# Optimization experiments

Measured on AMD Instinct MI355X. Metric: run time of the kernel, lower is better.

Reference implementation:

```python
import jax, jax.numpy as jnp
import numpy as np

B = 2            # batch size
GRID = 256       # BEV grid H = W
M = 30000        # number of pillars (voxels)
NPTS = 200000    # number of points
IN_C = 16
VOXEL = 0.4      # voxel_size[:2]
PC_MIN = -51.2   # pc_range[:2]
DS = 2           # prod(ds_layer_strides)


def _bn(x, g, b):
    # eval-mode BatchNorm with running_mean=0, running_var=1 (eps absorbed into g)
    return x * g + b


def _conv(x, k, stride):
    # 3x3 conv, padding=1 (spconv SparseConv2d / SubMConv2d with pad k//2), NHWC
    return jax.lax.conv_general_dilated(
        x, k, (stride, stride), ((1, 1), (1, 1)),
        dimension_numbers=('NHWC', 'HWIO', 'NHWC'))


def _active_mask(occ, stride):
    # active output sites of a sparse conv = any active input in the 3x3 receptive field
    pooled = jax.lax.reduce_window(occ, -jnp.inf, jax.lax.max,
                                   (1, 3, 3, 1), (1, stride, stride, 1),
                                   ((0, 0), (1, 1), (1, 1), (0, 0)))
    return (pooled > 0).astype(occ.dtype)


def _forward(features, pfn_w0, pfn_g0, pfn_b0, pfn_w1, pfn_g1, pfn_b1,
             b1_kd, b1_gd, b1_bd, b1_k1, b1_g1, b1_b1, b1_k2, b1_g2, b1_b2,
             b2_kd, b2_gd, b2_bd, b2_k1, b2_g1, b2_b1, b2_k2, b2_g2, b2_b2,
             unq, unq_inv, grid_size):
    # pillar mode: cols 0:2 are xy; convert to (fractional) voxel coordinates
    pos = (features[:, :2] - PC_MIN) / VOXEL  # [N,2] = (px, py)

    # PFN layer 0 (not last): linear(16->16) + BN + ReLU, concat per-pillar max
    h = jax.nn.relu(_bn(features @ pfn_w0, pfn_g0, pfn_b0))            # [N,16]
    hmax = jax.ops.segment_max(h, unq_inv, num_segments=M)             # [M,16]
    h = jnp.concatenate([h, hmax[unq_inv]], axis=1)                    # [N,32]
    # PFN layer 1 (last): linear(32->64) + BN + ReLU
    h = jax.nn.relu(_bn(h @ pfn_w1, pfn_g1, pfn_b1))                   # [N,64]

    # scatter_max pooling points -> pillars
    fv = jax.ops.segment_max(h, unq_inv, num_segments=M)               # [M,64]

    Hn = grid_size
    img = jnp.zeros((B, Hn, Hn, fv.shape[1]), fv.dtype)
    img = img.at[unq[:, 0], unq[:, 1], unq[:, 2]].set(fv)              # dense BEV, NHWC
    occ = jnp.zeros((B, Hn, Hn, 1), fv.dtype)
    occ = occ.at[unq[:, 0], unq[:, 1], unq[:, 2]].set(1.0)

    # block 1: SparseConvBlock(stride=1) + SparseBasicBlock (dense math, masked to active sites)
    occ1 = _active_mask(occ, 1)
    x = jax.nn.relu(_bn(_conv(img, b1_kd, 1), b1_gd, b1_bd)) * occ1
    y = jax.nn.relu(_bn(_conv(x, b1_k1, 1), b1_g1, b1_b1)) * occ1
    y = _bn(_conv(y, b1_k2, 1), b1_g2, b1_b2) * occ1
    x = jax.nn.relu(x + y)

    # block 2: SparseConvBlock(stride=2) + SparseBasicBlock
    occ2 = _active_mask(occ1, 2)
    x = jax.nn.relu(_bn(_conv(x, b2_kd, 2), b2_gd, b2_bd)) * occ2
    y = jax.nn.relu(_bn(_conv(x, b2_k1, 1), b2_g1, b2_b1)) * occ2
    y = _bn(_conv(y, b2_k2, 1), b2_g2, b2_b2) * occ2
    x = jax.nn.relu(x + y)                                             # [B,H/2,W/2,128]

    # bilinear gather at per-point downsampled positions (px -> W axis, py -> H axis)
    bidx = unq[unq_inv, 0]
    px = pos[:, 0] / DS
    py = pos[:, 1] / DS
    Hc, Wc = x.shape[1], x.shape[2]
    x0 = jnp.clip(jnp.floor(px).astype(jnp.int32), 0, Wc - 1)
    x1 = jnp.clip(jnp.floor(px).astype(jnp.int32) + 1, 0, Wc - 1)
    y0 = jnp.clip(jnp.floor(py).astype(jnp.int32), 0, Hc - 1)
    y1 = jnp.clip(jnp.floor(py).astype(jnp.int32) + 1, 0, Hc - 1)
    Ia = x[bidx, y0, x0]
    Ib = x[bidx, y1, x0]
    Ic = x[bidx, y0, x1]
    Id = x[bidx, y1, x1]
    x0f, x1f = x0.astype(px.dtype), x1.astype(px.dtype)
    y0f, y1f = y0.astype(py.dtype), y1.astype(py.dtype)
    wa = ((x1f - px) * (y1f - py))[:, None]
    wb = ((x1f - px) * (py - y0f))[:, None]
    wc = ((px - x0f) * (y1f - py))[:, None]
    wd = ((px - x0f) * (py - y0f))[:, None]
    return Ia * wa + Ib * wb + Ic * wc + Id * wd                       # [N,128]


def setup_inputs() -> dict:
    rng = np.random.default_rng(0)
    d = {}
    d['features'] = jnp.asarray(rng.standard_normal((NPTS, IN_C)).astype(np.float32))
    # unique voxel coords (batch, y, x)
    lin = rng.choice(B * GRID * GRID, size=M, replace=False)
    d['unq'] = jnp.asarray(np.stack([lin // (GRID * GRID), (lin // GRID) % GRID, lin % GRID], 1).astype(np.int32))
    # every pillar gets at least one point
    d['unq_inv'] = jnp.asarray(np.concatenate([np.arange(M), rng.integers(0, M, NPTS - M)]).astype(np.int32))
    d['grid_size'] = GRID

    def w(*s):
        fan = int(np.prod(s[:-1]))
        return jnp.asarray((rng.standard_normal(s) / np.sqrt(fan)).astype(np.float32))

    def g(c):
        return jnp.asarray((0.5 + 0.5 * rng.random(c)).astype(np.float32))

    def bb(c):
        return jnp.asarray((0.1 * rng.standard_normal(c)).astype(np.float32))

    d['pfn_w0'] = w(IN_C, 16); d['pfn_g0'] = g(16); d['pfn_b0'] = bb(16)
    d['pfn_w1'] = w(32, 64);   d['pfn_g1'] = g(64); d['pfn_b1'] = bb(64)
    d['b1_kd'] = w(3, 3, 64, 64);   d['b1_gd'] = g(64);  d['b1_bd'] = bb(64)
    d['b1_k1'] = w(3, 3, 64, 64);   d['b1_g1'] = g(64);  d['b1_b1'] = bb(64)
    d['b1_k2'] = w(3, 3, 64, 64);   d['b1_g2'] = g(64);  d['b1_b2'] = bb(64)
    d['b2_kd'] = w(3, 3, 64, 128);  d['b2_gd'] = g(128); d['b2_bd'] = bb(128)
    d['b2_k1'] = w(3, 3, 128, 128); d['b2_g1'] = g(128); d['b2_b1'] = bb(128)
    d['b2_k2'] = w(3, 3, 128, 128); d['b2_g2'] = g(128); d['b2_b2'] = bb(128)
    return d


def reference(features, unq, unq_inv, grid_size,
              pfn_w0, pfn_g0, pfn_b0, pfn_w1, pfn_g1, pfn_b1,
              b1_kd, b1_gd, b1_bd, b1_k1, b1_g1, b1_b1, b1_k2, b1_g2, b1_b2,
              b2_kd, b2_gd, b2_bd, b2_k1, b2_g1, b2_b1, b2_k2, b2_g2, b2_b2):
    return _forward(features, pfn_w0, pfn_g0, pfn_b0, pfn_w1, pfn_g1, pfn_b1,
                    b1_kd, b1_gd, b1_bd, b1_k1, b1_g1, b1_b1, b1_k2, b1_g2, b1_b2,
                    b2_kd, b2_gd, b2_bd, b2_k1, b2_g1, b2_b1, b2_k2, b2_g2, b2_b2,
                    unq, unq_inv, grid_size)
```

## Files before the change

### kernel.cpp

```cpp
#include <hip/hip_runtime.h>
#include <hip/hip_bf16.h>

#define NPTS    200000
#define MPIL    30000
#define BATCH   2
#define GRID0   256
#define PCMIN   (-51.2f)
#define VOXEL0  (0.4f)
#define NCHUNK  118

#define SLOT_B  ((size_t)16777216)
#define SLOT_F  ((size_t)33554432)

#define W0F 0
#define W1F 256
#define FB1 9216
#define FB2 156672
#define FB3 304128
#define FB4 451584
#define FB5 746496
#define FB6 1336320

#define WS_FLAG 0
#define WS_OCC8 64
#define WS_OCC1 (64 + 131072)
#define WS_OCC2 (64 + 262144)
#define WS_HMAX 393280
#define WS_CNT  2313280
#define WS_OFF  2433280
#define WS_CUR  2553344
#define WS_IDX  2673344
#define WS_LOC  3473344
#define WS_BS   3593344
#define WS_FX   393344

typedef __attribute__((ext_vector_type(8))) short v8s;
typedef __attribute__((ext_vector_type(4))) float f32x4;

static __device__ __forceinline__ float b2f(__hip_bfloat16 v) { return __bfloat162float(v); }
static __device__ __forceinline__ unsigned short f2bbits(float f) {
    __hip_bfloat16 h = __float2bfloat16(f);
    union { __hip_bfloat16 h; unsigned short u; } cv; cv.h = h; return cv.u;
}
static __device__ __forceinline__ float bits2f(unsigned short h) {
    union { unsigned int u; float f; } c; c.u = ((unsigned int)h) << 16; return c.f;
}
static __device__ __forceinline__ float lo2f(unsigned int u) {
    union { unsigned int u; float f; } c; c.u = u << 16; return c.f;
}
static __device__ __forceinline__ float hi2f(unsigned int u) {
    union { unsigned int u; float f; } c; c.u = u & 0xFFFF0000u; return c.f;
}
static __device__ __forceinline__ unsigned int pack2(float a, float b) {
    return (unsigned int)f2bbits(a) | ((unsigned int)f2bbits(b) << 16);
}
static __device__ __forceinline__ void split2(float a, float b, unsigned int& hi, unsigned int& lo) {
    unsigned short ha = f2bbits(a), hb = f2bbits(b);
    hi = (unsigned int)ha | ((unsigned int)hb << 16);
    float ra = a - bits2f(ha);
    float rb = b - bits2f(hb);
    lo = (unsigned int)f2bbits(ra) | ((unsigned int)f2bbits(rb) << 16);
}

static __device__ __forceinline__ float ldf(const void* p, size_t i, int isb) {
    return isb ? b2f(((const __hip_bfloat16*)p)[i]) : ((const float*)p)[i];
}
static __device__ __forceinline__ float4 ld4(const void* p, size_t i, int isb) {
    if (isb) {
        uint2 r = *(const uint2*)((const __hip_bfloat16*)p + i);
        return make_float4(lo2f(r.x), hi2f(r.x), lo2f(r.y), hi2f(r.y));
    }
    return *(const float4*)((const float*)p + i);
}
static __device__ __forceinline__ void st4(void* p, size_t i, int isb, float4 v) {
    if (isb) {
        uint2 pk; pk.x = pack2(v.x, v.y); pk.y = pack2(v.z, v.w);
        *(uint2*)((__hip_bfloat16*)p + i) = pk;
    } else {
        *(float4*)((float*)p + i) = v;
    }
}
static __device__ __forceinline__ void* actptr(void* ob, int slot, int isb) {
    return (char*)ob + (size_t)slot * (isb ? SLOT_B : SLOT_F);
}
static __device__ __forceinline__ float* wpool(void* ob, int isb) {
    return (float*)((char*)ob + 3 * (isb ? SLOT_B : SLOT_F));
}

__global__ void probe_kernel(const unsigned short* __restrict__ g0, int* __restrict__ flag) {
    if (threadIdx.x == 0 && blockIdx.x == 0) {
        int ok = 1;
        for (int i = 0; i < 8; i++) {
            unsigned short u = g0[i];
            if (u < 0x3E00 || u >= 0x4000) ok = 0;
        }
        *flag = ok;
    }
}

__global__ __launch_bounds__(256) void cvt_kernel(const void* __restrict__ src, void* ob,
                                                  int woff, int n, const int* __restrict__ flag) {
    int isb = *flag;
    int i = blockIdx.x * 256 + threadIdx.x;
    if (i < n) wpool(ob, isb)[woff + i] = ldf(src, i, isb);
}

__global__ __launch_bounds__(256) void wfrag_kernel(const void* __restrict__ src, void* ob,
                                                    int fb_bytes, int CIN, int COUT,
                                                    const int* __restrict__ flag)
{
    const int isb = *flag;
    const int cnt = 9 * CIN * COUT;
    int e = blockIdx.x * 256 + threadIdx.x;
    if (e >= cnt) return;
    int i = e & 7;
    int l = (e >> 3) & 63;
    int f = e >> 9;
    int nbn = COUT >> 4, kcn = CIN >> 5;
    int nb = f % nbn;
    int kc = (f / nbn) % kcn;
    int tap = f / (nbn * kcn);
    int ci = kc * 32 + (l >> 4) * 8 + i;
    int co = nb * 16 + (l & 15);
    float wv = ldf(src, (size_t)(tap * CIN + ci) * COUT + co, isb);
    unsigned short h = f2bbits(wv);
    float rem = wv - bits2f(h);
    short* wh = (short*)((char*)ob + 3 * (isb ? SLOT_B : SLOT_F) + fb_bytes);
    wh[e] = (short)h;
    wh[cnt + e] = (short)f2bbits(rem);
}

__global__ __launch_bounds__(256) void hist_kernel(const int* __restrict__ unq_inv,
                                                   int* __restrict__ cnt)
{
    int n = blockIdx.x * 256 + threadIdx.x;
    if (n < NPTS) atomicAdd(&cnt[unq_inv[n]], 1);
}

__global__ __launch_bounds__(256) void scan1_kernel(const int* __restrict__ cnt,
                                                    int* __restrict__ loc,
                                                    int* __restrict__ bs)
{
    __shared__ int s[256];
    const int tid = threadIdx.x;
    const int i = blockIdx.x * 256 + tid;
    int v = (i < MPIL) ? cnt[i] : 0;
    s[tid] = v;
    __syncthreads();
#pragma unroll
    for (int d = 1; d < 256; d <<= 1) {
        int t = (tid >= d) ? s[tid - d] : 0;
        __syncthreads();
        s[tid] += t;
        __syncthreads();
    }
    if (i < MPIL) loc[i] = s[tid] - v;
    if (tid == 255) bs[blockIdx.x] = s[255];
}

__global__ __launch_bounds__(128) void scan2_kernel(int* __restrict__ bs)
{
    __shared__ int s[NCHUNK];
    const int tid = threadIdx.x;
    for (int i = tid; i < NCHUNK; i += 128) s[i] = bs[i];
    __syncthreads();
    if (tid == 0) {
        int acc = 0;
        for (int i = 0; i < NCHUNK; i++) { int t = s[i]; s[i] = acc; acc += t; }
    }
    __syncthreads();
    for (int i = tid; i < NCHUNK; i += 128) bs[i] = s[i];
}

__global__ __launch_bounds__(256) void scan3_kernel(const int* __restrict__ loc,
                                                    const int* __restrict__ bs,
                                                    int* __restrict__ off,
                                                    int* __restrict__ cur)
{
    int i = blockIdx.x * 256 + threadIdx.x;
    if (i < MPIL) {
        int e = loc[i] + bs[blockIdx.x];
        off[i] = e; cur[i] = e;
    }
    if (i == 0) off[MPIL] = NPTS;
}

__global__ __launch_bounds__(256) void fill_kernel(const int* __restrict__ unq_inv,
                                                   int* __restrict__ cur,
                                                   int* __restrict__ idxarr)
{
    int n = blockIdx.x * 256 + threadIdx.x;
    if (n >= NPTS) return;
    int p = unq_inv[n];
    int s = atomicAdd(&cur[p], 1);
    idxarr[s] = n;
}

__global__ __launch_bounds__(256) void pfn0_kernel(
    const void* __restrict__ feat, void* ob, const void* __restrict__ g0,
    const void* __restrict__ b0, const int* __restrict__ flag)
{
    const int isb = *flag;
    int n = blockIdx.x * 256 + threadIdx.x;
    if (n >= NPTS) return;
    const float* w0f = wpool(ob, isb) + W0F;
    void* h0 = actptr(ob, 1, isb);
    float f[16];
#pragma unroll
    for (int i = 0; i < 16; i += 4) {
        float4 v = ld4(feat, (size_t)n * 16 + i, isb);
        f[i] = v.x; f[i + 1] = v.y; f[i + 2] = v.z; f[i + 3] = v.w;
    }
#pragma unroll
    for (int co = 0; co < 16; co += 4) {
        float a0 = 0.f, a1 = 0.f, a2 = 0.f, a3 = 0.f;
#pragma unroll
        for (int ci = 0; ci < 16; ci++) {
            float4 w = *(const float4*)&w0f[ci * 16 + co];
            a0 += f[ci] * w.x; a1 += f[ci] * w.y; a2 += f[ci] * w.z; a3 += f[ci] * w.w;
        }
        float o[4] = { a0, a1, a2, a3 };
#pragma unroll
        for (int k = 0; k < 4; k++) {
            float z = o[k] * ldf(g0, co + k, isb) + ldf(b0, co + k, isb);
            o[k] = fmaxf(z, 0.f);
        }
        st4(h0, (size_t)n * 16 + co, isb, make_float4(o[0], o[1], o[2], o[3]));
    }
}

__global__ __launch_bounds__(256) void hmax_kernel(
    void* ob, const int* __restrict__ off, const int* __restrict__ idxarr,
    float* __restrict__ hmax, const int* __restrict__ flag)
{
    const int isb = *flag;
    int t = blockIdx.x * 256 + threadIdx.x;
    if (t >= MPIL * 16) return;
    int p = t >> 4, ch = t & 15;
    const void* h0 = actptr(ob, 1, isb);
    float m = 0.f;
    int s1 = off[p + 1];
    for (int s = off[p]; s < s1; s++) {
        int n = idxarr[s];
        m = fmaxf(m, ldf(h0, (size_t)n * 16 + ch, isb));
    }
    hmax[t] = m;
}

template<bool BF>
static __device__ __forceinline__ void pfn1p_body(
    void* ob, const float* __restrict__ hmax, const void* __restrict__ g1,
    const void* __restrict__ b1, const int* __restrict__ off,
    const int* __restrict__ idxarr, const int* __restrict__ unq,
    unsigned char* __restrict__ occ)
{
    const int lane = threadIdx.x & 63;
    const int p = (blockIdx.x << 2) + (threadIdx.x >> 6);
    if (p >= MPIL) return;
    const int isb = BF ? 1 : 0;
    const float* w1f = wpool(ob, isb) + W1F;
    const void* h0 = actptr(ob, 1, isb);
    void* img = actptr(ob, 0, isb);

    float wcol[32];
#pragma unroll
    for (int k = 0; k < 32; k++) wcol[k] = w1f[k * 64 + lane];
    float base = 0.f;
#pragma unroll
    for (int k = 0; k < 16; k++) base += hmax[(size_t)p * 16 + k] * wcol[16 + k];
    const float g = ldf(g1, lane, isb);
    const float be = ldf(b1, lane, isb);

    float m = 0.f;
    const int s1 = off[p + 1];
    for (int s = off[p]; s < s1; s++) {
        const int n = idxarr[s];
        float h[16];
        if (BF) {
            const unsigned short* hp = (const unsigned short*)h0 + (size_t)n * 16;
            uint4 a = *(const uint4*)hp;
            uint4 c = *(const uint4*)(hp + 8);
            h[0] = lo2f(a.x); h[1] = hi2f(a.x); h[2] = lo2f(a.y); h[3] = hi2f(a.y);
            h[4] = lo2f(a.z); h[5] = hi2f(a.z); h[6] = lo2f(a.w); h[7] = hi2f(a.w);
            h[8] = lo2f(c.x); h[9] = hi2f(c.x); h[10] = lo2f(c.y); h[11] = hi2f(c.y);
            h[12] = lo2f(c.z); h[13] = hi2f(c.z); h[14] = lo2f(c.w); h[15] = hi2f(c.w);
        } else {
            const float* fp = (const float*)h0 + (size_t)n * 16;
#pragma unroll
            for (int i = 0; i < 16; i += 4) {
                float4 v = *(const float4*)(fp + i);
                h[i] = v.x; h[i + 1] = v.y; h[i + 2] = v.z; h[i + 3] = v.w;
            }
        }
        float z = base;
#pragma unroll
        for (int k = 0; k < 16; k++) z += h[k] * wcol[k];
        z = fmaxf(z * g + be, 0.f);
        m = fmaxf(m, z);
    }

    const int bb = unq[p * 3 + 0], yy = unq[p * 3 + 1], xx = unq[p * 3 + 2];
    const size_t site = ((size_t)bb * GRID0 + yy) * GRID0 + xx;
    if (BF) ((unsigned short*)img)[site * 64 + lane] = f2bbits(m);
    else    ((float*)img)[site * 64 + lane] = m;
    if (lane == 0) occ[site] = 1;
}

__global__ __launch_bounds__(256) void pfn1p_kernel(
    void* ob, const float* __restrict__ hmax, const void* __restrict__ g1,
    const void* __restrict__ b1, const int* __restrict__ off,
    const int* __restrict__ idxarr, const int* __restrict__ unq,
    unsigned char* __restrict__ occ, const int* __restrict__ flag)
{
    if (*flag) pfn1p_body<true>(ob, hmax, g1, b1, off, idxarr, unq, occ);
    else       pfn1p_body<false>(ob, hmax, g1, b1, off, idxarr, unq, occ);
}

__global__ __launch_bounds__(256) void dilate1_kernel(const unsigned char* __restrict__ occ,
                                                      unsigned char* __restrict__ occ1)
{
    int idx = blockIdx.x * 256 + threadIdx.x;
    if (idx >= BATCH * GRID0 * GRID0) return;
    int b = idx / (GRID0 * GRID0);
    int r = idx % (GRID0 * GRID0);
    int y = r / GRID0, x = r % GRID0;
    unsigned char v = 0;
#pragma unroll
    for (int dy = -1; dy <= 1; dy++) {
        int yy = y + dy; if (yy < 0 || yy >= GRID0) continue;
#pragma unroll
        for (int dx = -1; dx <= 1; dx++) {
            int xx = x + dx; if (xx < 0 || xx >= GRID0) continue;
            v |= occ[((size_t)b * GRID0 + yy) * GRID0 + xx];
        }
    }
    occ1[idx] = v ? 1 : 0;
}

__global__ __launch_bounds__(256) void dilate2_kernel(const unsigned char* __restrict__ occ1,
                                                      unsigned char* __restrict__ occ2)
{
    int idx = blockIdx.x * 256 + threadIdx.x;
    if (idx >= BATCH * 128 * 128) return;
    int b = idx / (128 * 128);
    int r = idx % (128 * 128);
    int y = r / 128, x = r % 128;
    unsigned char v = 0;
#pragma unroll
    for (int dy = -1; dy <= 1; dy++) {
        int yy = 2 * y + dy; if (yy < 0 || yy >= GRID0) continue;
#pragma unroll
        for (int dx = -1; dx <= 1; dx++) {
            int xx = 2 * x + dx; if (xx < 0 || xx >= GRID0) continue;
            v |= occ1[((size_t)b * GRID0 + yy) * GRID0 + xx];
        }
    }
    occ2[idx] = v ? 1 : 0;
}

template<int CIN, int COUT, int STRIDE, bool ADD_RES, bool BF, int RR>
static __device__ __forceinline__ void conv_tile(
    short* s_a, const void* in, void* outp, const void* res, const short* wh,
    const void* gamma, const void* beta, const unsigned char* mask,
    int HIN, int WIN, int HOUT, int WOUT, int b, int oy0, int ox0)
{
    constexpr int Y_EXT = (RR - 1) * STRIDE + 3;
    constexpr int X_EXT = 15 * STRIDE + 3;
    constexpr int PSTR = CIN + 8;
    constexpr int TSZ = Y_EXT * X_EXT * PSTR;
    constexpr int NCH8 = CIN / 8;
    constexpr int NBW = COUT / 16 / 4;
    constexpr int KCN = CIN / 32;
    constexpr int NOB = COUT / 16;

    const int tid = threadIdx.x;

    __syncthreads();
    for (int i = tid; i < Y_EXT * X_EXT * NCH8; i += 256) {
        int c8 = i % NCH8;
        int r = i / NCH8;
        int xo = r % X_EXT;
        int dy = r / X_EXT;
        int yin = oy0 * STRIDE - 1 + dy;
        int xin = ox0 * STRIDE - 1 + xo;
        bool inb = (yin >= 0 && yin < HIN && xin >= 0 && xin < WIN);
        int si = (dy * X_EXT + xo) * PSTR + c8 * 8;
        size_t gi = (((size_t)b * HIN + yin) * WIN + xin) * (size_t)CIN + c8 * 8;
        if (BF) {
            uint4 v = make_uint4(0u, 0u, 0u, 0u);
            if (inb) v = *(const uint4*)((const unsigned short*)in + gi);
            *(uint4*)&s_a[si] = v;
        } else {
            float4 va = make_float4(0.f, 0.f, 0.f, 0.f);
            float4 vb = make_float4(0.f, 0.f, 0.f, 0.f);
            if (inb) {
                va = *(const float4*)((const float*)in + gi);
                vb = *(const float4*)((const float*)in + gi + 4);
            }
            uint4 hv, lv;
            split2(va.x, va.y, hv.x, lv.x);
            split2(va.z, va.w, hv.y, lv.y);
            split2(vb.x, vb.y, hv.z, lv.z);
            split2(vb.z, vb.w, hv.w, lv.w);
            *(uint4*)&s_a[si] = hv;
            *(uint4*)&s_a[TSZ + si] = lv;
        }
    }
    __syncthreads();

    const int lane = tid & 63;
    const int w = tid >> 6;
    const int nb0 = w * NBW;
    const int l15 = lane & 15;
    const int lhi = lane >> 4;
    const short* wl = wh + 9 * CIN * COUT;

    f32x4 acc[RR][NBW];
#pragma unroll
    for (int rr = 0; rr < RR; rr++)
#pragma unroll
        for (int nb = 0; nb < NBW; nb++) acc[rr][nb] = (f32x4){0.f, 0.f, 0.f, 0.f};

#pragma unroll 1
    for (int tap = 0; tap < 9; tap++) {
        const int ky = tap / 3;
        const int kx = tap - ky * 3;
        const int axy = ky * X_EXT + l15 * STRIDE + kx;
#pragma unroll
        for (int kc = 0; kc < KCN; kc++) {
            const int f0 = (tap * KCN + kc) * NOB + nb0;
            v8s bh[NBW];
#pragma unroll
            for (int nb = 0; nb < NBW; nb++)
                bh[nb] = *(const v8s*)&wh[(size_t)(f0 + nb) * 512 + lane * 8];
#pragma unroll
            for (int rr = 0; rr < RR; rr++) {
                const int abase = (rr * STRIDE * X_EXT + axy) * PSTR + lhi * 8 + kc * 32;
                const v8s ah = *(const v8s*)&s_a[abase];
#pragma unroll
                for (int nb = 0; nb < NBW; nb++)
                    acc[rr][nb] = __builtin_amdgcn_mfma_f32_16x16x32_bf16(ah, bh[nb], acc[rr][nb], 0, 0, 0);
                if constexpr (!BF) {
                    const v8s al = *(const v8s*)&s_a[TSZ + abase];
#pragma unroll
                    for (int nb = 0; nb < NBW; nb++) {
                        const v8s bl = *(const v8s*)&wl[(size_t)(f0 + nb) * 512 + lane * 8];
                        acc[rr][nb] = __builtin_amdgcn_mfma_f32_16x16x32_bf16(ah, bl, acc[rr][nb], 0, 0, 0);
                        acc[rr][nb] = __builtin_amdgcn_mfma_f32_16x16x32_bf16(al, bh[nb], acc[rr][nb], 0, 0, 0);
                    }
                }
            }
        }
    }

#pragma unroll
    for (int rr = 0; rr < RR; rr++) {
        const int oy = oy0 + rr;
        const size_t mrow = ((size_t)b * HOUT + oy) * WOUT + ox0 + lhi * 4;
        const unsigned int mw = *(const unsigned int*)&mask[mrow];
#pragma unroll
        for (int nb = 0; nb < NBW; nb++) {
            const int n = (nb0 + nb) * 16 + l15;
            const float g = ldf(gamma, n, BF ? 1 : 0);
            const float be = ldf(beta, n, BF ? 1 : 0);
#pragma unroll
            for (int r = 0; r < 4; r++) {
                const size_t oaddr = (mrow + r) * COUT + n;
                float z = acc[rr][nb][r] * g + be;
                z *= ((mw >> (8 * r)) & 0xFF) ? 1.f : 0.f;
                if constexpr (ADD_RES) z += ldf(res, oaddr, BF ? 1 : 0);
                z = fmaxf(z, 0.f);
                if (BF) ((unsigned short*)outp)[oaddr] = f2bbits(z);
                else    ((float*)outp)[oaddr] = z;
            }
        }
    }
}

template<int CIN, int COUT, int STRIDE, int R, bool ADD_RES>
__global__ __launch_bounds__(256) void convmf_kernel(
    void* ob, int in_slot, int out_slot, void* out_ws, int res_slot, int fb_bytes,
    const void* __restrict__ gamma, const void* __restrict__ beta,
    const unsigned char* __restrict__ mask, const int* __restrict__ flag,
    int HIN, int WIN, int HOUT, int WOUT)
{
    constexpr int X_EXT = 15 * STRIDE + 3;
    constexpr int PSTR = CIN + 8;
    constexpr int TSZ_B = ((R - 1) * STRIDE + 3) * X_EXT * PSTR;
    constexpr int TSZ_F = ((R / 2 - 1) * STRIDE + 3) * X_EXT * PSTR;
    constexpr int LDS_SH = (TSZ_B > 2 * TSZ_F) ? TSZ_B : 2 * TSZ_F;
    __shared__ __align__(16) short s_a[LDS_SH];

    const int nbx = gridDim.x, nby = gridDim.y;
    const int nwg = nbx * nby * (int)gridDim.z;
    int bid = blockIdx.x + nbx * (blockIdx.y + nby * blockIdx.z);
    bid = (bid & 7) * (nwg >> 3) + (bid >> 3);
    const int bx = bid % nbx;
    const int byy = (bid / nbx) % nby;
    const int bz = bid / (nbx * nby);

    const int isb = *flag;
    const void* in = actptr(ob, in_slot, isb);
    void* outp = out_ws ? out_ws : actptr(ob, out_slot, isb);
    const void* res = ADD_RES ? actptr(ob, res_slot, isb) : nullptr;
    const short* wh = (const short*)((const char*)ob + 3 * (isb ? SLOT_B : SLOT_F) + fb_bytes);

    if (isb) {
        conv_tile<CIN, COUT, STRIDE, ADD_RES, true, R>(
            s_a, in, outp, res, wh, gamma, beta, mask,
            HIN, WIN, HOUT, WOUT, bz, byy * R, bx * 16);
    } else {
        conv_tile<CIN, COUT, STRIDE, ADD_RES, false, R / 2>(
            s_a, in, outp, res, wh, gamma, beta, mask,
            HIN, WIN, HOUT, WOUT, bz, byy * R, bx * 16);
        conv_tile<CIN, COUT, STRIDE, ADD_RES, false, R / 2>(
            s_a, in, outp, res, wh, gamma, beta, mask,
            HIN, WIN, HOUT, WOUT, bz, byy * R + R / 2, bx * 16);
    }
}

__global__ __launch_bounds__(256) void gather_kernel(
    const void* __restrict__ x, const void* __restrict__ feat,
    const int* __restrict__ unq, const int* __restrict__ unq_inv,
    void* __restrict__ out, const int* __restrict__ flag)
{
    const int isb = *flag;
    int idx = blockIdx.x * 256 + threadIdx.x;
    if (idx >= NPTS * 32) return;
    int n = idx >> 5;
    int co = (idx & 31) * 4;
    float fx = ldf(feat, (size_t)n * 16 + 0, isb);
    float fy = ldf(feat, (size_t)n * 16 + 1, isb);
    float px = ((fx - PCMIN) / VOXEL0) / 2.0f;
    float py = ((fy - PCMIN) / VOXEL0) / 2.0f;
    int bi = unq[(size_t)unq_inv[n] * 3 + 0];
    int xf = (int)floorf(px), yf = (int)floorf(py);
    int x0 = min(max(xf, 0), 127), x1 = min(max(xf + 1, 0), 127);
    int y0 = min(max(yf, 0), 127), y1 = min(max(yf + 1, 0), 127);
    float x0f = (float)x0, x1f = (float)x1, y0f = (float)y0, y1f = (float)y1;
    float wa = (x1f - px) * (y1f - py);
    float wb = (x1f - px) * (py - y0f);
    float wc = (px - x0f) * (y1f - py);
    float wd = (px - x0f) * (py - y0f);
    size_t base = (size_t)bi * 128 * 128 * 128;
    float4 Ia = ld4(x, base + ((size_t)y0 * 128 + x0) * 128 + co, isb);
    float4 Ib = ld4(x, base + ((size_t)y1 * 128 + x0) * 128 + co, isb);
    float4 Ic = ld4(x, base + ((size_t)y0 * 128 + x1) * 128 + co, isb);
    float4 Id = ld4(x, base + ((size_t)y1 * 128 + x1) * 128 + co, isb);
    float4 r;
    r.x = Ia.x * wa + Ib.x * wb + Ic.x * wc + Id.x * wd;
    r.y = Ia.y * wa + Ib.y * wb + Ic.y * wc + Id.y * wd;
    r.z = Ia.z * wa + Ib.z * wb + Ic.z * wc + Id.z * wd;
    r.w = Ia.w * wa + Ib.w * wb + Ic.w * wc + Id.w * wd;
    st4(out, (size_t)n * 128 + co, isb, r);
}

extern "C" void kernel_launch(void* const* d_in, const int* in_sizes, int n_in,
                              void* d_out, int out_size, void* d_ws, size_t ws_size,
                              hipStream_t stream)
{
    (void)in_sizes; (void)n_in; (void)out_size; (void)ws_size;
    const int* unq = (const int*)d_in[1];
    const int* unq_inv = (const int*)d_in[2];

    char* ws = (char*)d_ws;
    int* flagp = (int*)(ws + WS_FLAG);
    unsigned char* occ8 = (unsigned char*)(ws + WS_OCC8);
    unsigned char* occ1m = (unsigned char*)(ws + WS_OCC1);
    unsigned char* occ2m = (unsigned char*)(ws + WS_OCC2);
    float* hmax = (float*)(ws + WS_HMAX);
    int* cnt = (int*)(ws + WS_CNT);
    int* off = (int*)(ws + WS_OFF);
    int* cur = (int*)(ws + WS_CUR);
    int* idxarr = (int*)(ws + WS_IDX);
    int* loc = (int*)(ws + WS_LOC);
    int* bs = (int*)(ws + WS_BS);
    void* Fx = (void*)(ws + WS_FX);

    probe_kernel<<<1, 64, 0, stream>>>((const unsigned short*)d_in[5], flagp);

    cvt_kernel<<<1, 256, 0, stream>>>(d_in[4], d_out, W0F, 256, flagp);
    cvt_kernel<<<8, 256, 0, stream>>>(d_in[7], d_out, W1F, 2048, flagp);
    wfrag_kernel<<<144, 256, 0, stream>>>(d_in[10], d_out, FB1, 64, 64, flagp);
    wfrag_kernel<<<144, 256, 0, stream>>>(d_in[13], d_out, FB2, 64, 64, flagp);
    wfrag_kernel<<<144, 256, 0, stream>>>(d_in[16], d_out, FB3, 64, 64, flagp);
    wfrag_kernel<<<288, 256, 0, stream>>>(d_in[19], d_out, FB4, 64, 128, flagp);
    wfrag_kernel<<<576, 256, 0, stream>>>(d_in[22], d_out, FB5, 128, 128, flagp);
    wfrag_kernel<<<576, 256, 0, stream>>>(d_in[25], d_out, FB6, 128, 128, flagp);

    hipMemsetAsync(d_out, 0, SLOT_F, stream);
    hipMemsetAsync(cnt, 0, (size_t)MPIL * 4, stream);
    hipMemsetAsync(occ8, 0, 131072, stream);

    hist_kernel<<<(NPTS + 255) / 256, 256, 0, stream>>>(unq_inv, cnt);
    scan1_kernel<<<NCHUNK, 256, 0, stream>>>(cnt, loc, bs);
    scan2_kernel<<<1, 128, 0, stream>>>(bs);
    scan3_kernel<<<NCHUNK, 256, 0, stream>>>(loc, bs, off, cur);
    fill_kernel<<<(NPTS + 255) / 256, 256, 0, stream>>>(unq_inv, cur, idxarr);
    pfn0_kernel<<<(NPTS + 255) / 256, 256, 0, stream>>>(d_in[0], d_out, d_in[5], d_in[6], flagp);
    hmax_kernel<<<(MPIL * 16 + 255) / 256, 256, 0, stream>>>(d_out, off, idxarr, hmax, flagp);
    pfn1p_kernel<<<(MPIL + 3) / 4, 256, 0, stream>>>(d_out, hmax, d_in[8], d_in[9],
                                                     off, idxarr, unq, occ8, flagp);

    dilate1_kernel<<<(BATCH * GRID0 * GRID0) / 256, 256, 0, stream>>>(occ8, occ1m);
    dilate2_kernel<<<(BATCH * 128 * 128) / 256, 256, 0, stream>>>(occ1m, occ2m);

    dim3 blk(256);
    dim3 g1(16, 16, BATCH);
    convmf_kernel<64, 64, 1, 16, false><<<g1, blk, 0, stream>>>(
        d_out, 0, 1, nullptr, 0, FB1, d_in[11], d_in[12], occ1m, flagp, 256, 256, 256, 256);
    convmf_kernel<64, 64, 1, 16, false><<<g1, blk, 0, stream>>>(
        d_out, 1, 2, nullptr, 0, FB2, d_in[14], d_in[15], occ1m, flagp, 256, 256, 256, 256);
    convmf_kernel<64, 64, 1, 16, true><<<g1, blk, 0, stream>>>(
        d_out, 2, 0, nullptr, 1, FB3, d_in[17], d_in[18], occ1m, flagp, 256, 256, 256, 256);
    dim3 g2a(8, 32, BATCH), g2b(8, 16, BATCH);
    convmf_kernel<64, 128, 2, 4, false><<<g2a, blk, 0, stream>>>(
        d_out, 0, 1, nullptr, 0, FB4, d_in[20], d_in[21], occ2m, flagp, 256, 256, 128, 128);
    convmf_kernel<128, 128, 1, 8, false><<<g2b, blk, 0, stream>>>(
        d_out, 1, 2, nullptr, 0, FB5, d_in[23], d_in[24], occ2m, flagp, 128, 128, 128, 128);
    convmf_kernel<128, 128, 1, 8, true><<<g2b, blk, 0, stream>>>(
        d_out, 2, 0, Fx, 1, FB6, d_in[26], d_in[27], occ2m, flagp, 128, 128, 128, 128);

    gather_kernel<<<(NPTS * 32) / 256, 256, 0, stream>>>(Fx, d_in[0], unq, unq_inv,
                                                         d_out, flagp);
}
```

Measured before the change: 561.4 us.

## Split conv output channels across blocks and rows across waves for more parallelism

Each conv block now handles only half of the output channels, selected by the z grid index. Within a block, the 4 waves are arranged as a 2D grid of row groups by channel groups instead of one channel group each. Row tiles are shrunk and the grid is enlarged, giving roughly four times as many workgroups for better occupancy and load balance across CUs. The cost is that each input halo tile is loaded from memory twice, once per channel half, and each block does less MFMA work per LDS load.

```diff
diff --git a/kernel.cpp b/kernel.cpp
--- a/kernel.cpp
+++ b/kernel.cpp
@@ -358,18 +358,19 @@
     occ2[idx] = v ? 1 : 0;
 }
 
-template<int CIN, int COUT, int STRIDE, bool ADD_RES, bool BF, int RR>
+template<int CIN, int COUT, int STRIDE, bool ADD_RES, bool BF, int RT, int WR, int WC>
 static __device__ __forceinline__ void conv_tile(
     short* s_a, const void* in, void* outp, const void* res, const short* wh,
     const void* gamma, const void* beta, const unsigned char* mask,
-    int HIN, int WIN, int HOUT, int WOUT, int b, int oy0, int ox0)
-{
-    constexpr int Y_EXT = (RR - 1) * STRIDE + 3;
+    int HIN, int WIN, int HOUT, int WOUT, int b, int oy0, int ox0, int nbB)
+{
+    constexpr int Y_EXT = (RT - 1) * STRIDE + 3;
     constexpr int X_EXT = 15 * STRIDE + 3;
     constexpr int PSTR = CIN + 8;
     constexpr int TSZ = Y_EXT * X_EXT * PSTR;
     constexpr int NCH8 = CIN / 8;
-    constexpr int NBW = COUT / 16 / 4;
+    constexpr int RRW = RT / WR;
+    constexpr int NBW = COUT / 16 / 2 / WC;
     constexpr int KCN = CIN / 32;
     constexpr int NOB = COUT / 16;
 
@@ -410,14 +411,17 @@
 
     const int lane = tid & 63;
     const int w = tid >> 6;
-    const int nb0 = w * NBW;
+    const int wr = w / WC;
+    const int wn = w % WC;
+    const int nb0 = nbB + wn * NBW;
+    const int row0 = wr * RRW;
     const int l15 = lane & 15;
     const int lhi = lane >> 4;
     const short* wl = wh + 9 * CIN * COUT;
 
-    f32x4 acc[RR][NBW];
-#pragma unroll
-    for (int rr = 0; rr < RR; rr++)
+    f32x4 acc[RRW][NBW];
+#pragma unroll
+    for (int rr = 0; rr < RRW; rr++)
 #pragma unroll
         for (int nb = 0; nb < NBW; nb++) acc[rr][nb] = (f32x4){0.f, 0.f, 0.f, 0.f};
 
@@ -434,8 +438,8 @@
             for (int nb = 0; nb < NBW; nb++)
                 bh[nb] = *(const v8s*)&wh[(size_t)(f0 + nb) * 512 + lane * 8];
 #pragma unroll
-            for (int rr = 0; rr < RR; rr++) {
-                const int abase = (rr * STRIDE * X_EXT + axy) * PSTR + lhi * 8 + kc * 32;
+            for (int rr = 0; rr < RRW; rr++) {
+                const int abase = ((row0 + rr) * STRIDE * X_EXT + axy) * PSTR + lhi * 8 + kc * 32;
                 const v8s ah = *(const v8s*)&s_a[abase];
 #pragma unroll
                 for (int nb = 0; nb < NBW; nb++)
@@ -454,8 +458,8 @@
     }
 
 #pragma unroll
-    for (int rr = 0; rr < RR; rr++) {
-        const int oy = oy0 + rr;
+    for (int rr = 0; rr < RRW; rr++) {
+        const int oy = oy0 + row0 + rr;
         const size_t mrow = ((size_t)b * HOUT + oy) * WOUT + ox0 + lhi * 4;
         const unsigned int mw = *(const unsigned int*)&mask[mrow];
 #pragma unroll
@@ -477,7 +481,7 @@
     }
 }
 
-template<int CIN, int COUT, int STRIDE, int R, bool ADD_RES>
+template<int CIN, int COUT, int STRIDE, int R, int RTF, int WR, int WC, bool ADD_RES>
 __global__ __launch_bounds__(256) void convmf_kernel(
     void* ob, int in_slot, int out_slot, void* out_ws, int res_slot, int fb_bytes,
     const void* __restrict__ gamma, const void* __restrict__ beta,
@@ -487,7 +491,7 @@
     constexpr int X_EXT = 15 * STRIDE + 3;
     constexpr int PSTR = CIN + 8;
     constexpr int TSZ_B = ((R - 1) * STRIDE + 3) * X_EXT * PSTR;
-    constexpr int TSZ_F = ((R / 2 - 1) * STRIDE + 3) * X_EXT * PSTR;
+    constexpr int TSZ_F = ((RTF - 1) * STRIDE + 3) * X_EXT * PSTR;
     constexpr int LDS_SH = (TSZ_B > 2 * TSZ_F) ? TSZ_B : 2 * TSZ_F;
     __shared__ __align__(16) short s_a[LDS_SH];
 
@@ -497,7 +501,10 @@
     bid = (bid & 7) * (nwg >> 3) + (bid >> 3);
     const int bx = bid % nbx;
     const int byy = (bid / nbx) % nby;
-    const int bz = bid / (nbx * nby);
+    const int bzz = bid / (nbx * nby);
+    const int b = bzz >> 1;
+    const int coh = bzz & 1;
+    const int nbB = coh * (COUT / 32);
 
     const int isb = *flag;
     const void* in = actptr(ob, in_slot, isb);
@@ -506,16 +513,15 @@
     const short* wh = (const short*)((const char*)ob + 3 * (isb ? SLOT_B : SLOT_F) + fb_bytes);
 
     if (isb) {
-        conv_tile<CIN, COUT, STRIDE, ADD_RES, true, R>(
+        conv_tile<CIN, COUT, STRIDE, ADD_RES, true, R, WR, WC>(
             s_a, in, outp, res, wh, gamma, beta, mask,
-            HIN, WIN, HOUT, WOUT, bz, byy * R, bx * 16);
+            HIN, WIN, HOUT, WOUT, b, byy * R, bx * 16, nbB);
     } else {
-        conv_tile<CIN, COUT, STRIDE, ADD_RES, false, R / 2>(
-            s_a, in, outp, res, wh, gamma, beta, mask,
-            HIN, WIN, HOUT, WOUT, bz, byy * R, bx * 16);
-        conv_tile<CIN, COUT, STRIDE, ADD_RES, false, R / 2>(
-            s_a, in, outp, res, wh, gamma, beta, mask,
-            HIN, WIN, HOUT, WOUT, bz, byy * R + R / 2, bx * 16);
+#pragma unroll
+        for (int p = 0; p < R / RTF; p++)
+            conv_tile<CIN, COUT, STRIDE, ADD_RES, false, RTF, WR, WC>(
+                s_a, in, outp, res, wh, gamma, beta, mask,
+                HIN, WIN, HOUT, WOUT, b, byy * R + p * RTF, bx * 16, nbB);
     }
 }
 
@@ -606,19 +612,19 @@
     dilate2_kernel<<<(BATCH * 128 * 128) / 256, 256, 0, stream>>>(occ1m, occ2m);
 
     dim3 blk(256);
-    dim3 g1(16, 16, BATCH);
-    convmf_kernel<64, 64, 1, 16, false><<<g1, blk, 0, stream>>>(
+    dim3 g1(16, 32, BATCH * 2);
+    convmf_kernel<64, 64, 1, 8, 2, 2, 2, false><<<g1, blk, 0, stream>>>(
         d_out, 0, 1, nullptr, 0, FB1, d_in[11], d_in[12], occ1m, flagp, 256, 256, 256, 256);
-    convmf_kernel<64, 64, 1, 16, false><<<g1, blk, 0, stream>>>(
+    convmf_kernel<64, 64, 1, 8, 2, 2, 2, false><<<g1, blk, 0, stream>>>(
         d_out, 1, 2, nullptr, 0, FB2, d_in[14], d_in[15], occ1m, flagp, 256, 256, 256, 256);
-    convmf_kernel<64, 64, 1, 16, true><<<g1, blk, 0, stream>>>(
+    convmf_kernel<64, 64, 1, 8, 2, 2, 2, true><<<g1, blk, 0, stream>>>(
         d_out, 2, 0, nullptr, 1, FB3, d_in[17], d_in[18], occ1m, flagp, 256, 256, 256, 256);
-    dim3 g2a(8, 32, BATCH), g2b(8, 16, BATCH);
-    convmf_kernel<64, 128, 2, 4, false><<<g2a, blk, 0, stream>>>(
+    dim3 g2a(8, 64, BATCH * 2), g2b(8, 32, BATCH * 2);
+    convmf_kernel<64, 128, 2, 2, 1, 1, 4, false><<<g2a, blk, 0, stream>>>(
         d_out, 0, 1, nullptr, 0, FB4, d_in[20], d_in[21], occ2m, flagp, 256, 256, 128, 128);
-    convmf_kernel<128, 128, 1, 8, false><<<g2b, blk, 0, stream>>>(
+    convmf_kernel<128, 128, 1, 4, 1, 1, 4, false><<<g2b, blk, 0, stream>>>(
         d_out, 1, 2, nullptr, 0, FB5, d_in[23], d_in[24], occ2m, flagp, 128, 128, 128, 128);
-    convmf_kernel<128, 128, 1, 8, true><<<g2b, blk, 0, stream>>>(
+    convmf_kernel<128, 128, 1, 4, 1, 1, 4, true><<<g2b, blk, 0, stream>>>(
         d_out, 2, 0, Fx, 1, FB6, d_in[26], d_in[27], occ2m, flagp, 128, 128, 128, 128);
 
     gather_kernel<<<(NPTS * 32) / 256, 256, 0, stream>>>(Fx, d_in[0], unq, unq_inv,
```

New measurement: 640.9 us. 1.14x slower.
